# Performance work log

Hardware: AMD Instinct MI355X
Metric: run time of the kernel (lower is better)

## Reference

```python
import jax, jax.numpy as jnp
import numpy as np

IN_FEATURES = 1024
OUT_FEATURES = 256
NUM_KNOTS = 10
SPLINE_ORDER = 3
NUM_BASIS = NUM_KNOTS + SPLINE_ORDER  # 13
EPS = 1e-8


def setup_inputs() -> dict:
    key = jax.random.key(0)
    k1, k2 = jax.random.split(key)
    x = jax.random.normal(k1, (8192, IN_FEATURES), dtype=jnp.float32)
    spline_coeffs = jax.random.normal(
        k2, (OUT_FEATURES, IN_FEATURES, NUM_BASIS), dtype=jnp.float32) * 0.1
    knots = jnp.linspace(-1.0, 1.0, NUM_KNOTS + 2 * SPLINE_ORDER, dtype=jnp.float32)
    return {"x": x, "spline_coeffs": spline_coeffs, "knots": knots}


def _basis_functions(x, knots):
    # x: (B, I) already tanh-normalized; returns (B, I, NUM_BASIS)
    xc = jnp.clip(x, -1.0, 1.0)[..., None]          # (B, I, 1)
    left = knots[:NUM_BASIS - 1]                     # (nb-1,)
    center = knots[1:NUM_BASIS]                      # (nb-1,)
    right = knots[2:NUM_BASIS + 1]                   # (nb-1,)  (i+2 < len(knots) always)
    mask_l = (xc >= left) & (xc < center)
    mask_r = (xc >= center) & (xc < right)
    up = mask_l.astype(xc.dtype) * (xc - left) / (center - left + EPS)
    down = mask_r.astype(xc.dtype) * (right - xc) / (right - center + EPS)
    b = up + down                                    # (B, I, nb-1)
    # last basis column is never written in the original loop -> zeros
    return jnp.pad(b, ((0, 0), (0, 0), (0, 1)))


def reference(x, spline_coeffs, knots):
    x_norm = jnp.tanh(x)
    basis = _basis_functions(x_norm, knots)          # (B, I, K)
    # output[b, j] = sum_i sum_k basis[b, i, k] * coeffs[j, i, k]
    return jnp.einsum('bik,jik->bj', basis, spline_coeffs)
```

## Files before the change

### kernel.cpp

```cpp
#include <hip/hip_runtime.h>
#include <cstdint>
#include <cstddef>


typedef _Float16 half2_v __attribute__((ext_vector_type(2)));
typedef __fp16  fp16x2  __attribute__((ext_vector_type(2)));
typedef _Float16 f16x8 __attribute__((ext_vector_type(8)));
typedef float f32x4 __attribute__((ext_vector_type(4)));

__device__ __forceinline__ half2_v u32_as_h2(uint32_t u) {
  union { uint32_t u; half2_v h; } c; c.u = u; return c.h;
}
__device__ __forceinline__ uint32_t h2_as_u32(half2_v h) {
  union { uint32_t u; half2_v h; } c; c.h = h; return c.u;
}
__device__ __forceinline__ half2_v cvt_pk_h2(float a, float b) {
  union { fp16x2 f; half2_v h; } c;
  c.f = __builtin_amdgcn_cvt_pkrtz(a, b);
  return c.h;
}
__device__ __forceinline__ float dot2f(half2_v a, half2_v b, float c) {
#if __has_builtin(__builtin_amdgcn_fdot2)
  return __builtin_amdgcn_fdot2(a, b, c, false);
#else
  return c + (float)a[0] * (float)b[0] + (float)a[1] * (float)b[1];
#endif
}
__device__ __forceinline__ uint16_t f16_bits(float v) {
  union { _Float16 h; uint16_t u; } c; c.h = (_Float16)v; return c.u;
}

__device__ __forceinline__ float fast_tanhf(float v) {
  const float e = __expf(2.0f * v);
  return 1.0f - 2.0f / (e + 1.0f);
}

#define KSTEP 0.13333333333333333f
#define KINV  7.49999943750004f
__device__ __forceinline__ void kan_weights(float xin, float& w0, float& w1, int& lo) {
  float xc = fast_tanhf(xin);
  xc = fminf(fmaxf(xc, -1.0f), 1.0f);
  int m = (int)((xc + 1.0f) * 7.5f);
  m = min(max(m, 0), 14);
  const float k0 = fmaf((float)m, KSTEP, -1.0f);
  const float up = (xc - k0) * KINV;
  const float dn = (k0 + KSTEP - xc) * KINV;
  w0 = (m == 0) ? up : ((m <= 12) ? dn : 0.0f);
  w1 = (m >= 1 && m <= 11) ? up : 0.0f;
  lo = min(max(m - 1, 0), 11);
}

__device__ __forceinline__ void load_lds16(const void* g, void* l) {
  __builtin_amdgcn_global_load_lds((const __attribute__((address_space(1))) void*)g,
                                   (__attribute__((address_space(3))) void*)l, 16, 0, 0);
}

#define GMM 8192
#define GNN 256
#define KI  16
#define GK2 (1024 * KI)
#define KSPL2 4
#define IPER (1024 / KSPL2)
#define BM2 128
#define BN2 128
#define NIT (IPER / 4)

__global__ __launch_bounds__(256)
void kan_prep_B2(const float* __restrict__ coef, uint32_t* __restrict__ B2) {
  const int tid = blockIdx.x * 256 + threadIdx.x;
  const float* cp = coef + (size_t)tid * 13;
  uint32_t w[8];
#pragma unroll
  for (int q = 0; q < 6; ++q) w[q] = h2_as_u32(cvt_pk_h2(cp[2 * q], cp[2 * q + 1]));
  w[6] = 0u; w[7] = 0u;
  uint4* p = (uint4*)(B2 + (size_t)tid * 8);
  p[0] = make_uint4(w[0], w[1], w[2], w[3]);
  p[1] = make_uint4(w[4], w[5], w[6], w[7]);
}

__global__ __launch_bounds__(256)
void kan_gemm6(const float* __restrict__ x, const _Float16* __restrict__ B2,
               float* __restrict__ out) {
  __shared__ __align__(16) char Bs[2][BN2 * 128];
  __shared__ __align__(16) char As[2][4 * 128 * 32];

  const int t    = threadIdx.x;
  const int lane = t & 63;
  const int wv   = t >> 6;
  const int mw   = wv & 1;
  const int nw   = wv >> 1;
  const int fr   = lane & 15;
  const int fq   = lane >> 4;
  const int m0   = blockIdx.x * BM2;
  const int n0   = blockIdx.y * BN2;
  const int i00  = blockIdx.z * IPER;

  f32x4 acc[4][4];
#pragma unroll
  for (int a = 0; a < 4; ++a)
#pragma unroll
    for (int b = 0; b < 4; ++b) acc[a][b] = (f32x4){0.f, 0.f, 0.f, 0.f};

  const int sn[4] = { (0 * 256 + t) >> 3, (1 * 256 + t) >> 3,
                      (2 * 256 + t) >> 3, (3 * 256 + t) >> 3 };
  const int sc = t & 7;
  const int p_row = t & 127;
  const int p_ip  = (t >> 7) * 2;
  const float* xrow = x + (size_t)(m0 + p_row) * 1024 + p_ip;

  auto stageB = [&](int it) {
    const _Float16* Bb = B2 + (size_t)(i00 + it * 4) * KI;
    char* Bd = (char*)Bs[it & 1];
#pragma unroll
    for (int s = 0; s < 4; ++s) {
      const int c = sc ^ (sn[s] & 7);
      load_lds16(Bb + (size_t)(n0 + sn[s]) * GK2 + c * 8, Bd + (s * 256 + t) * 16);
    }
  };
  auto loadx = [&](int it) -> float2 {
    return *(const float2*)(xrow + i00 + it * 4);
  };
  auto expand = [&](int it, float2 xv) {
    char* Ab = As[it & 1];
#pragma unroll
    for (int d = 0; d < 2; ++d) {
      float w0, w1; int lo;
      kan_weights(d ? xv.y : xv.x, w0, w1, lo);
      const uint32_t wp  = (uint32_t)f16_bits(w0) | ((uint32_t)f16_bits(w1) << 16);
      const uint32_t wlo = (lo & 1) ? (wp << 16) : wp;
      const uint32_t whi = (lo & 1) ? (wp >> 16) : 0u;
      uint32_t* r = (uint32_t*)(Ab + (size_t)((p_ip + d) * 128 + p_row) * 32);
      *(uint4*)(r)     = make_uint4(0u, 0u, 0u, 0u);
      *(uint4*)(r + 4) = make_uint4(0u, 0u, 0u, 0u);
      r[(lo >> 1) + 1] = whi;
      r[lo >> 1]       = wlo;
    }
  };

  float2 xc = loadx(0);
  stageB(0);
  expand(0, xc);
  float2 xn = loadx(1);

  for (int it = 0; it < NIT; ++it) {
    __syncthreads();

    if (it + 1 < NIT) {
      stageB(it + 1);
      expand(it + 1, xn);
      if (it + 2 < NIT) xn = loadx(it + 2);
    }

    const char* Bd = (const char*)Bs[it & 1];
    const char* Ad = (const char*)As[it & 1];
#pragma unroll
    for (int ks = 0; ks < 2; ++ks) {
      const int iloc = ks * 2 + (fq >> 1);
      f16x8 af[4];
#pragma unroll
      for (int mi = 0; mi < 4; ++mi)
        af[mi] = *(const f16x8*)(Ad +
                   ((iloc * 128 + mw * 64 + mi * 16 + fr) * 32 + (fq & 1) * 16));
#pragma unroll
      for (int ni = 0; ni < 4; ++ni) {
        const int row = nw * 64 + ni * 16 + fr;
        const int col = ks * 4 + fq;
        const f16x8 bf = *(const f16x8*)(Bd + (row * 8 + (col ^ (row & 7))) * 16);
#pragma unroll
        for (int mi = 0; mi < 4; ++mi)
          acc[mi][ni] = __builtin_amdgcn_mfma_f32_16x16x32_f16(af[mi], bf, acc[mi][ni], 0, 0, 0);
      }
    }
  }

#pragma unroll
  for (int mi = 0; mi < 4; ++mi) {
    const int gr = m0 + mw * 64 + mi * 16 + fq * 4;
#pragma unroll
    for (int ni = 0; ni < 4; ++ni) {
      const int gc = n0 + nw * 64 + ni * 16 + fr;
#pragma unroll
      for (int r = 0; r < 4; ++r)
        atomicAdd(&out[(size_t)(gr + r) * GNN + gc], acc[mi][ni][r]);
    }
  }
}

#define TI 8
#define BT 256
#define JT 32
#define ISPL 2
#define IRANGE (1024 / ISPL)

__global__ __launch_bounds__(256)
void kan_dot2(const float* __restrict__ x, const float* __restrict__ coef,
              float* __restrict__ out) {
  __shared__ uint32_t Plds[TI * 12 * JT];
  const int t    = threadIdx.x;
  const int b    = blockIdx.x * BT + t;
  const int j0   = blockIdx.y * JT;
  const int cbeg = blockIdx.z * (IRANGE / TI);

  float acc[JT];
#pragma unroll
  for (int q = 0; q < JT; ++q) acc[q] = 0.0f;

  const int s_jj   = t & 31;
  const int s_iloc = t >> 5;

  for (int c = cbeg; c < cbeg + IRANGE / TI; ++c) {
    const int i0 = c * TI;
    __syncthreads();
    {
      const float* cp0 = coef + ((size_t)(j0 + s_jj) * 1024 + (i0 + s_iloc)) * 13;
      float cv[13];
#pragma unroll
      for (int s = 0; s < 13; ++s) cv[s] = cp0[s];
#pragma unroll
      for (int r = 0; r < 12; ++r) {
        half2_v h; h[0] = (_Float16)cv[r]; h[1] = (_Float16)cv[r + 1];
        const int slot = ((s_jj >> 2) + r) & 7;
        Plds[(s_iloc * 12 + r) * 32 + slot * 4 + (s_jj & 3)] = h2_as_u32(h);
      }
    }
    uint32_t wr[TI]; int lor[TI];
    {
      const float* xr = x + (size_t)b * 1024 + i0;
      const float4 xa = *(const float4*)(xr);
      const float4 xb = *(const float4*)(xr + 4);
      const float xv[TI] = {xa.x, xa.y, xa.z, xa.w, xb.x, xb.y, xb.z, xb.w};
#pragma unroll
      for (int q = 0; q < TI; ++q) {
        float w0, w1; int lo;
        kan_weights(xv[q], w0, w1, lo);
        wr[q] = (uint32_t)f16_bits(w0) | ((uint32_t)f16_bits(w1) << 16);
        lor[q] = lo;
      }
    }
    __syncthreads();

    const uint4* P4 = (const uint4*)Plds;
#pragma unroll
    for (int ii = 0; ii < TI; ++ii) {
      const half2_v hw = u32_as_h2(wr[ii]);
      const int lo = lor[ii];
      const int base = (ii * 12 + lo) * 8;
#pragma unroll
      for (int g = 0; g < 8; ++g) {
        const uint4 v = P4[base + ((g + lo) & 7)];
        acc[4 * g + 0] = dot2f(hw, u32_as_h2(v.x), acc[4 * g + 0]);
        acc[4 * g + 1] = dot2f(hw, u32_as_h2(v.y), acc[4 * g + 1]);
        acc[4 * g + 2] = dot2f(hw, u32_as_h2(v.z), acc[4 * g + 2]);
        acc[4 * g + 3] = dot2f(hw, u32_as_h2(v.w), acc[4 * g + 3]);
      }
    }
  }

  float* orow = out + (size_t)b * 256 + j0;
#pragma unroll
  for (int q = 0; q < JT; ++q) atomicAdd(orow + q, acc[q]);
}

extern "C" void kernel_launch(void* const* d_in, const int* in_sizes, int n_in,
                              void* d_out, int out_size, void* d_ws, size_t ws_size,
                              hipStream_t stream) {
  const float* x     = (const float*)d_in[0];
  const float* coef  = (const float*)d_in[1];
  float* out = (float*)d_out;

  (void)hipMemsetAsync(out, 0, (size_t)out_size * sizeof(float), stream);

  const size_t nB2 = (size_t)GNN * GK2;
  if (ws_size >= nB2 * 2) {
    _Float16* B2 = (_Float16*)d_ws;
    kan_prep_B2<<<(int)((size_t)GNN * 1024 / 256), 256, 0, stream>>>(coef, (uint32_t*)B2);
    dim3 grid(GMM / BM2, GNN / BN2, KSPL2);
    kan_gemm6<<<grid, 256, 0, stream>>>(x, B2, out);
  } else {
    dim3 grid(8192 / BT, 256 / JT, ISPL);
    kan_dot2<<<grid, 256, 0, stream>>>(x, coef, out);
  }
}
```

Measured before the change: 197.3 us.

## Enlarge GEMM tile to 256x256 with 512 threads, deeper split-K and swizzled A LDS

Replaces the 128x128, 256-thread GEMM with a 256x256 tile using 512 threads (8 waves), so each block covers all 256 output columns. Split-K goes from 4 to 8 and the grid is reordered so K-splits of the same row block are adjacent. It also adds an XOR swizzle on the expanded A tile in LDS to reduce bank conflicts, and reorders the inner loop to hold B fragments in registers. The aim is to remove redundant x loads and basis expansion across N tiles and to raise MFMA reuse. The cost is more accumulator registers (128 floats per thread), more LDS per block, and twice the atomic output traffic from the deeper split-K.

```diff
diff --git a/kernel.cpp b/kernel.cpp
--- a/kernel.cpp
+++ b/kernel.cpp
@@ -59,10 +59,10 @@
 #define GNN 256
 #define KI  16
 #define GK2 (1024 * KI)
-#define KSPL2 4
+#define KSPL2 8
 #define IPER (1024 / KSPL2)
-#define BM2 128
-#define BN2 128
+#define BM2 256
+#define BN2 256
 #define NIT (IPER / 4)
 
 __global__ __launch_bounds__(256)
@@ -78,11 +78,11 @@
   p[1] = make_uint4(w[4], w[5], w[6], w[7]);
 }
 
-__global__ __launch_bounds__(256)
-void kan_gemm6(const float* __restrict__ x, const _Float16* __restrict__ B2,
+__global__ __launch_bounds__(512, 2)
+void kan_gemm7(const float* __restrict__ x, const _Float16* __restrict__ B2,
                float* __restrict__ out) {
   __shared__ __align__(16) char Bs[2][BN2 * 128];
-  __shared__ __align__(16) char As[2][4 * 128 * 32];
+  __shared__ __align__(16) char As[2][4 * BM2 * 32];
 
   const int t    = threadIdx.x;
   const int lane = t & 63;
@@ -91,21 +91,23 @@
   const int nw   = wv >> 1;
   const int fr   = lane & 15;
   const int fq   = lane >> 4;
-  const int m0   = blockIdx.x * BM2;
-  const int n0   = blockIdx.y * BN2;
-  const int i00  = blockIdx.z * IPER;
-
-  f32x4 acc[4][4];
-#pragma unroll
-  for (int a = 0; a < 4; ++a)
+  const int m0   = blockIdx.z * BM2;
+  const int i00  = blockIdx.x * IPER;
+  const int fr_swz = ((fr >> 2) & 1) * 16;
+  const int a_half = (fq & 1) * 16;
+
+  f32x4 acc[8][4];
+#pragma unroll
+  for (int a = 0; a < 8; ++a)
 #pragma unroll
     for (int b = 0; b < 4; ++b) acc[a][b] = (f32x4){0.f, 0.f, 0.f, 0.f};
 
-  const int sn[4] = { (0 * 256 + t) >> 3, (1 * 256 + t) >> 3,
-                      (2 * 256 + t) >> 3, (3 * 256 + t) >> 3 };
+  const int sn[4] = { (0 * 512 + t) >> 3, (1 * 512 + t) >> 3,
+                      (2 * 512 + t) >> 3, (3 * 512 + t) >> 3 };
   const int sc = t & 7;
-  const int p_row = t & 127;
-  const int p_ip  = (t >> 7) * 2;
+  const int p_row = t & 255;
+  const int p_ip  = (t >> 8) * 2;
+  const int p_swz = ((p_row >> 2) & 1) * 16;
   const float* xrow = x + (size_t)(m0 + p_row) * 1024 + p_ip;
 
   auto stageB = [&](int it) {
@@ -114,7 +116,7 @@
 #pragma unroll
     for (int s = 0; s < 4; ++s) {
       const int c = sc ^ (sn[s] & 7);
-      load_lds16(Bb + (size_t)(n0 + sn[s]) * GK2 + c * 8, Bd + (s * 256 + t) * 16);
+      load_lds16(Bb + (size_t)sn[s] * GK2 + c * 8, Bd + (s * 512 + t) * 16);
     }
   };
   auto loadx = [&](int it) -> float2 {
@@ -129,11 +131,12 @@
       const uint32_t wp  = (uint32_t)f16_bits(w0) | ((uint32_t)f16_bits(w1) << 16);
       const uint32_t wlo = (lo & 1) ? (wp << 16) : wp;
       const uint32_t whi = (lo & 1) ? (wp >> 16) : 0u;
-      uint32_t* r = (uint32_t*)(Ab + (size_t)((p_ip + d) * 128 + p_row) * 32);
-      *(uint4*)(r)     = make_uint4(0u, 0u, 0u, 0u);
-      *(uint4*)(r + 4) = make_uint4(0u, 0u, 0u, 0u);
-      r[(lo >> 1) + 1] = whi;
-      r[lo >> 1]       = wlo;
+      const int w = lo >> 1;
+      char* rb = Ab + (size_t)((p_ip + d) * BM2 + p_row) * 32;
+      *(uint4*)(rb + p_swz)        = make_uint4(0u, 0u, 0u, 0u);
+      *(uint4*)(rb + (p_swz ^ 16)) = make_uint4(0u, 0u, 0u, 0u);
+      *(uint32_t*)(rb + (((w + 1) * 4) ^ p_swz)) = whi;
+      *(uint32_t*)(rb + ((w * 4) ^ p_swz))       = wlo;
     }
   };
 
@@ -156,29 +159,29 @@
 #pragma unroll
     for (int ks = 0; ks < 2; ++ks) {
       const int iloc = ks * 2 + (fq >> 1);
-      f16x8 af[4];
-#pragma unroll
-      for (int mi = 0; mi < 4; ++mi)
-        af[mi] = *(const f16x8*)(Ad +
-                   ((iloc * 128 + mw * 64 + mi * 16 + fr) * 32 + (fq & 1) * 16));
+      f16x8 bf[4];
 #pragma unroll
       for (int ni = 0; ni < 4; ++ni) {
         const int row = nw * 64 + ni * 16 + fr;
-        const int col = ks * 4 + fq;
-        const f16x8 bf = *(const f16x8*)(Bd + (row * 8 + (col ^ (row & 7))) * 16);
-#pragma unroll
-        for (int mi = 0; mi < 4; ++mi)
-          acc[mi][ni] = __builtin_amdgcn_mfma_f32_16x16x32_f16(af[mi], bf, acc[mi][ni], 0, 0, 0);
-      }
-    }
-  }
-
-#pragma unroll
-  for (int mi = 0; mi < 4; ++mi) {
-    const int gr = m0 + mw * 64 + mi * 16 + fq * 4;
+        bf[ni] = *(const f16x8*)(Bd + (row * 8 + ((ks * 4 + fq) ^ (row & 7))) * 16);
+      }
+#pragma unroll
+      for (int mi = 0; mi < 8; ++mi) {
+        const f16x8 af = *(const f16x8*)(Ad +
+            (size_t)((iloc * BM2 + mw * 128 + mi * 16 + fr) * 32) + (a_half ^ fr_swz));
+#pragma unroll
+        for (int ni = 0; ni < 4; ++ni)
+          acc[mi][ni] = __builtin_amdgcn_mfma_f32_16x16x32_f16(af, bf[ni], acc[mi][ni], 0, 0, 0);
+      }
+    }
+  }
+
+#pragma unroll
+  for (int mi = 0; mi < 8; ++mi) {
+    const int gr = m0 + mw * 128 + mi * 16 + fq * 4;
 #pragma unroll
     for (int ni = 0; ni < 4; ++ni) {
-      const int gc = n0 + nw * 64 + ni * 16 + fr;
+      const int gc = nw * 64 + ni * 16 + fr;
 #pragma unroll
       for (int r = 0; r < 4; ++r)
         atomicAdd(&out[(size_t)(gr + r) * GNN + gc], acc[mi][ni][r]);
@@ -274,8 +277,8 @@
   if (ws_size >= nB2 * 2) {
     _Float16* B2 = (_Float16*)d_ws;
     kan_prep_B2<<<(int)((size_t)GNN * 1024 / 256), 256, 0, stream>>>(coef, (uint32_t*)B2);
-    dim3 grid(GMM / BM2, GNN / BN2, KSPL2);
-    kan_gemm6<<<grid, 256, 0, stream>>>(x, B2, out);
+    dim3 grid(KSPL2, 1, GMM / BM2);
+    kan_gemm7<<<grid, 512, 0, stream>>>(x, B2, out);
   } else {
     dim3 grid(8192 / BT, 256 / JT, ISPL);
     kan_dot2<<<grid, 256, 0, stream>>>(x, coef, out);
```

Result: no change. 194.0 us (-1.7%).
